# Kernel tuning notes

Hardware: AMD Instinct MI355X
Metric: run time of the kernel (lower is better)

Reference implementation:

```python
import jax, jax.numpy as jnp
import numpy as np

H, DH, C, K = 8, 128, 200, 15  # heads, head_dim, context_size, conv kernel
SCALE = DH ** -0.5
EPS = 1e-5


def layernorm(x, g, b):
    mu = jnp.mean(x, axis=-1, keepdims=True)
    var = jnp.mean(jnp.square(x - mu), axis=-1, keepdims=True)
    return (x - mu) * jax.lax.rsqrt(var + EPS) * g + b


def feedforward(x, ln_g, ln_b, up_w, up_b, down_w, down_b):
    h = layernorm(x, ln_g, ln_b)
    h = jax.nn.silu(h @ up_w + up_b)
    return h @ down_w + down_b


def attention(x, dist, ln_g, ln_b, wq, wkv, wo, wo_b, rel_emb):
    h = layernorm(x, ln_g, ln_b)
    b, f, d = h.shape
    nb = f // C  # num_features chosen divisible by context_size (no remainder path)
    q = (h @ wq).reshape(b, nb, C, H, DH).transpose(0, 1, 3, 2, 4)   # [b,nb,H,C,dh]
    kv = h @ wkv
    k, v = jnp.split(kv, 2, axis=-1)
    k = k.reshape(b, nb, C, H, DH).transpose(0, 1, 3, 2, 4)
    v = v.reshape(b, nb, C, H, DH).transpose(0, 1, 3, 2, 4)
    rel = rel_emb[dist]                                              # [C,C,dh]
    pos_attn = jnp.einsum('bnhid,ijd->bnhij', q, rel) * SCALE
    scores = jnp.einsum('bnhid,bnhjd->bnhij', q, k) * SCALE + pos_attn
    probs = jax.nn.softmax(scores, axis=-1)
    out = jnp.einsum('bnhij,bnhjd->bnhid', probs, v)
    out = out.transpose(0, 1, 3, 2, 4).reshape(b, f, H * DH)
    return out @ wo + wo_b


def conv_module(x, ln_g, ln_b, up_w, up_b, dw_w, bn_g, bn_b, bn_mean, bn_var, down_w, down_b):
    h = layernorm(x, ln_g, ln_b)
    h = h @ up_w + up_b                         # pointwise conv == linear; [b,L,2*inner]
    a, gate = jnp.split(h, 2, axis=-1)
    h = a * jax.nn.sigmoid(gate)                # GLU over channel dim
    h = h.transpose(0, 2, 1)                    # [b,inner,L]
    pad = K // 2
    h = jax.lax.conv_general_dilated(
        h, dw_w[:, None, :], window_strides=(1,), padding=[(pad, pad)],
        dimension_numbers=('NCH', 'OIH', 'NCH'), feature_group_count=h.shape[1])
    # BatchNorm1d in eval mode (running stats)
    h = (h - bn_mean[None, :, None]) * jax.lax.rsqrt(bn_var[None, :, None] + EPS)
    h = h * bn_g[None, :, None] + bn_b[None, :, None]
    h = jax.nn.silu(h)
    h = h.transpose(0, 2, 1) @ down_w + down_b  # [b,L,hidden]
    return h


def block_forward(x, attention_dists,
                  ff1_ln_g, ff1_ln_b, ff1_up_w, ff1_up_b, ff1_down_w, ff1_down_b,
                  attn_ln_g, attn_ln_b, wq, wkv, wo, wo_b, rel_emb,
                  conv_ln_g, conv_ln_b, conv_up_w, conv_up_b, dw_w,
                  bn_g, bn_b, bn_mean, bn_var, conv_down_w, conv_down_b,
                  ff2_ln_g, ff2_ln_b, ff2_up_w, ff2_up_b, ff2_down_w, ff2_down_b,
                  post_ln_g, post_ln_b):
    x = 0.5 * feedforward(x, ff1_ln_g, ff1_ln_b, ff1_up_w, ff1_up_b, ff1_down_w, ff1_down_b) + x
    x = attention(x, attention_dists, attn_ln_g, attn_ln_b, wq, wkv, wo, wo_b, rel_emb) + x
    x = conv_module(x, conv_ln_g, conv_ln_b, conv_up_w, conv_up_b, dw_w,
                    bn_g, bn_b, bn_mean, bn_var, conv_down_w, conv_down_b) + x
    x = 0.5 * feedforward(x, ff2_ln_g, ff2_ln_b, ff2_up_w, ff2_up_b, ff2_down_w, ff2_down_b) + x
    return layernorm(x, post_ln_g, post_ln_b)


def setup_inputs() -> dict:
    key = jax.random.key(0)
    ks = iter(jax.random.split(key, 40))
    d, dff, inner = 1024, 4096, 2048
    r = lambda shape, s=0.02: (jax.random.normal(next(ks), shape, jnp.float32) * s)
    inp = {
        'x': jax.random.normal(next(ks), (8, 2000, d), jnp.float32),
        'attention_dists': jax.random.randint(next(ks), (C, C), 0, 1025, jnp.int32),
        'ff1_ln_g': jnp.ones((d,)), 'ff1_ln_b': jnp.zeros((d,)),
        'ff1_up_w': r((d, dff)), 'ff1_up_b': jnp.zeros((dff,)),
        'ff1_down_w': r((dff, d)), 'ff1_down_b': jnp.zeros((d,)),
        'attn_ln_g': jnp.ones((d,)), 'attn_ln_b': jnp.zeros((d,)),
        'wq': r((d, H * DH)), 'wkv': r((d, 2 * H * DH)),
        'wo': r((H * DH, d)), 'wo_b': jnp.zeros((d,)),
        'rel_emb': r((2 * 512 + 1, DH)),
        'conv_ln_g': jnp.ones((d,)), 'conv_ln_b': jnp.zeros((d,)),
        'conv_up_w': r((d, 2 * inner)), 'conv_up_b': jnp.zeros((2 * inner,)),
        'dw_w': r((inner, K)),
        'bn_g': jnp.ones((inner,)), 'bn_b': jnp.zeros((inner,)),
        'bn_mean': r((inner,)), 'bn_var': jax.random.uniform(next(ks), (inner,), jnp.float32) + 0.5,
        'conv_down_w': r((inner, d)), 'conv_down_b': jnp.zeros((d,)),
        'ff2_ln_g': jnp.ones((d,)), 'ff2_ln_b': jnp.zeros((d,)),
        'ff2_up_w': r((d, dff)), 'ff2_up_b': jnp.zeros((dff,)),
        'ff2_down_w': r((dff, d)), 'ff2_down_b': jnp.zeros((d,)),
        'post_ln_g': jnp.ones((d,)), 'post_ln_b': jnp.zeros((d,)),
    }
    return inp


def reference(x, attention_dists,
              ff1_ln_g, ff1_ln_b, ff1_up_w, ff1_up_b, ff1_down_w, ff1_down_b,
              attn_ln_g, attn_ln_b, wq, wkv, wo, wo_b, rel_emb,
              conv_ln_g, conv_ln_b, conv_up_w, conv_up_b, dw_w,
              bn_g, bn_b, bn_mean, bn_var, conv_down_w, conv_down_b,
              ff2_ln_g, ff2_ln_b, ff2_up_w, ff2_up_b, ff2_down_w, ff2_down_b,
              post_ln_g, post_ln_b):
    return block_forward(x, attention_dists,
                         ff1_ln_g, ff1_ln_b, ff1_up_w, ff1_up_b, ff1_down_w, ff1_down_b,
                         attn_ln_g, attn_ln_b, wq, wkv, wo, wo_b, rel_emb,
                         conv_ln_g, conv_ln_b, conv_up_w, conv_up_b, dw_w,
                         bn_g, bn_b, bn_mean, bn_var, conv_down_w, conv_down_b,
                         ff2_ln_g, ff2_ln_b, ff2_up_w, ff2_up_b, ff2_down_w, ff2_down_b,
                         post_ln_g, post_ln_b)
```

## Files before the change

kernel.cpp:

```cpp
#include <hip/hip_runtime.h>

typedef unsigned short u16;
typedef unsigned int u32;
using short8 = __attribute__((ext_vector_type(8))) short;
using floatx4 = __attribute__((ext_vector_type(4))) float;

#define DMODEL 1024
#define DFF 4096
#define INNER 2048
#define DH 128
#define CTX 200
#define R_TOT 16000
#define ABN 40
#define AROWS (ABN * CTX)
#define AM (ABN * 8)
#define SCALE_Q 0.08838834764831845f

__device__ __forceinline__ u16 f2bf(float f) {
    union { float f; u32 u; } v; v.f = f;
    u32 r = v.u + 0x7FFFu + ((v.u >> 16) & 1u);
    return (u16)(r >> 16);
}
__device__ __forceinline__ float bf2f(u16 u) {
    union { u32 u; float f; } v; v.u = ((u32)u) << 16; return v.f;
}
__device__ __forceinline__ float sigmoidf_(float x) { return 1.f / (1.f + __expf(-x)); }

__device__ __forceinline__ void load_lds16(const void* g, void* l) {
    __builtin_amdgcn_global_load_lds((const __attribute__((address_space(1))) u32*)g,
                                     (__attribute__((address_space(3))) u32*)l, 16, 0, 0);
}

template <typename RowMap>
__device__ __forceinline__ void stage256(const char* __restrict__ src, RowMap rowoff, int nrows,
                                         int row0, int k0b, char* dst) {
    const int lane = threadIdx.x & 63;
    const int wave = threadIdx.x >> 6;
#pragma unroll
    for (int r = 0; r < 4; ++r) {
        int o = r * 8192 + wave * 1024 + lane * 16;
        int row = o >> 7;
        int srcb = (o & 127) ^ ((row & 7) << 4);
        int grow = row0 + row;
        grow = (grow < nrows) ? grow : (nrows - 1);
        const char* g = src + rowoff(grow) + k0b + srcb;
        load_lds16(g, dst + r * 8192 + wave * 1024);
    }
}

template <typename RMA, typename RMB, typename Epi>
__device__ __forceinline__ void gemm256_core(const char* __restrict__ A, RMA rma, int a_rows,
                                             const char* __restrict__ B, RMB rmb, int b_rows,
                                             int K, int row0, int col0, char* lds, Epi epi) {
    const int lane = threadIdx.x & 63;
    const int wave = threadIdx.x >> 6;
    const int wrow = (wave >> 2) * 128;
    const int wcol = (wave & 3) * 64;
    const int lr = lane & 15;
    const int kg = lane >> 4;
    const int nt = K >> 6;

    floatx4 acc[8][4];
#pragma unroll
    for (int i = 0; i < 8; ++i)
#pragma unroll
        for (int j = 0; j < 4; ++j) acc[i][j] = (floatx4){0.f, 0.f, 0.f, 0.f};

    stage256(A, rma, a_rows, row0, 0, lds);
    stage256(B, rmb, b_rows, col0, 0, lds + 32768);
    asm volatile("s_waitcnt vmcnt(0)" ::: "memory");
    __builtin_amdgcn_s_barrier();

    for (int t = 0; t < nt; ++t) {
        char* cur = lds + (t & 1) * 65536;
        char* nxt = lds + ((t + 1) & 1) * 65536;
        if (t + 1 < nt) {
            stage256(A, rma, a_rows, row0, (t + 1) << 7, nxt);
            stage256(B, rmb, b_rows, col0, (t + 1) << 7, nxt + 32768);
        }
#pragma unroll
        for (int ks = 0; ks < 2; ++ks) {
            short8 av[8], bv[4];
#pragma unroll
            for (int mi = 0; mi < 8; ++mi) {
                int row = wrow + mi * 16 + lr;
                int cb = (ks * 64 + kg * 16) ^ ((row & 7) << 4);
                av[mi] = *(const short8*)(cur + row * 128 + cb);
            }
#pragma unroll
            for (int ni = 0; ni < 4; ++ni) {
                int row = wcol + ni * 16 + lr;
                int cb = (ks * 64 + kg * 16) ^ ((row & 7) << 4);
                bv[ni] = *(const short8*)(cur + 32768 + row * 128 + cb);
            }
            __builtin_amdgcn_s_setprio(1);
#pragma unroll
            for (int mi = 0; mi < 8; ++mi)
#pragma unroll
                for (int ni = 0; ni < 4; ++ni)
                    acc[mi][ni] = __builtin_amdgcn_mfma_f32_16x16x32_bf16(av[mi], bv[ni],
                                                                          acc[mi][ni], 0, 0, 0);
            __builtin_amdgcn_s_setprio(0);
        }
        if (t + 1 < nt)
            asm volatile("s_waitcnt vmcnt(0) lgkmcnt(0)" ::: "memory");
        else
            asm volatile("s_waitcnt lgkmcnt(0)" ::: "memory");
        __builtin_amdgcn_sched_barrier(0);
        __builtin_amdgcn_s_barrier();
    }
#pragma unroll
    for (int mi = 0; mi < 8; ++mi)
#pragma unroll
        for (int ni = 0; ni < 4; ++ni)
#pragma unroll
            for (int rr = 0; rr < 4; ++rr)
                epi(row0 + wrow + mi * 16 + kg * 4 + rr, col0 + wcol + ni * 16 + lr,
                    acc[mi][ni][rr]);
}

__device__ __forceinline__ void xcd_stripe_remap(int& bx, int& by) {
    const int gx = gridDim.x;
    const int gxs = gx >> 3;
    const int id = blockIdx.y * gx + blockIdx.x;
    const int xcd = id & 7;
    const int local = id >> 3;
    bx = xcd * gxs + (local % gxs);
    by = local / gxs;
}

template <int MODE>
__global__ __launch_bounds__(512, 2) void k_gemm256(const u16* __restrict__ A, int lda,
                                                    const u16* __restrict__ Bt, int ldb,
                                                    const float* __restrict__ bias, float alpha,
                                                    void* out, int ldc, const float* resid,
                                                    int M, int N, int K) {
    __shared__ __align__(128) char lds[131072];
    int bx, by;
    xcd_stripe_remap(bx, by);
    const int row0 = bx * 256, col0 = by * 256;
    if (row0 >= M) return;
    u16* ob = (u16*)out;
    float* of = (float*)out;
    const size_t la = (size_t)lda * 2, lb = (size_t)ldb * 2;
    gemm256_core((const char*)A, [=](int r) { return (size_t)r * la; }, M,
                 (const char*)Bt, [=](int r) { return (size_t)r * lb; }, N, K, row0, col0, lds,
                 [&](int r, int c, float v) {
                     if (r >= M) return;
                     size_t idx = (size_t)r * ldc + c;
                     float bb = bias ? bias[c] : 0.f;
                     if (MODE == 0) {
                         ob[idx] = f2bf(alpha * v + bb);
                     } else if (MODE == 1) {
                         float t = v + bb;
                         ob[idx] = f2bf(t * sigmoidf_(t));
                     } else {
                         of[idx] = alpha * (v + bb) + resid[idx];
                     }
                 });
}

template <typename RowMap>
__device__ __forceinline__ void stage_tile_g(const char* __restrict__ src, RowMap rowoff,
                                             int nrows, int row0, int k0b, char* tile) {
    const int lane = threadIdx.x & 63;
    const int wave = threadIdx.x >> 6;
#pragma unroll
    for (int r = 0; r < 4; ++r) {
        int o = r * 4096 + wave * 1024 + lane * 16;
        int row = o >> 7;
        int srcb = (o & 127) ^ ((row & 7) << 4);
        int grow = row0 + row;
        grow = (grow < nrows) ? grow : (nrows - 1);
        const char* g = src + rowoff(grow) + k0b + srcb;
        load_lds16(g, tile + r * 4096 + wave * 1024);
    }
}

template <typename RMA, typename RMB, typename Epi>
__device__ __forceinline__ void gemm_core_g(const char* __restrict__ A, RMA rma, int a_rows,
                                            const char* __restrict__ B, RMB rmb, int b_rows,
                                            int K, int row0, int col0, char* lds, Epi epi) {
    const int lane = threadIdx.x & 63;
    const int wave = threadIdx.x >> 6;
    const int wrow = (wave >> 1) * 64;
    const int wcol = (wave & 1) * 64;
    const int lr = lane & 15;
    const int kg = lane >> 4;
    const int nt = K >> 6;

    floatx4 acc[4][4];
#pragma unroll
    for (int i = 0; i < 4; ++i)
#pragma unroll
        for (int j = 0; j < 4; ++j) acc[i][j] = (floatx4){0.f, 0.f, 0.f, 0.f};

    stage_tile_g(A, rma, a_rows, row0, 0, lds);
    stage_tile_g(B, rmb, b_rows, col0, 0, lds + 16384);
    asm volatile("s_waitcnt vmcnt(0)" ::: "memory");
    __builtin_amdgcn_s_barrier();

    for (int t = 0; t < nt; ++t) {
        char* cur = lds + (t & 1) * 32768;
        char* nxt = lds + ((t + 1) & 1) * 32768;
        if (t + 1 < nt) {
            stage_tile_g(A, rma, a_rows, row0, (t + 1) << 7, nxt);
            stage_tile_g(B, rmb, b_rows, col0, (t + 1) << 7, nxt + 16384);
        }
#pragma unroll
        for (int ks = 0; ks < 2; ++ks) {
            short8 av[4], bv[4];
#pragma unroll
            for (int mi = 0; mi < 4; ++mi) {
                int row = wrow + mi * 16 + lr;
                int cb = (ks * 64 + kg * 16) ^ ((row & 7) << 4);
                av[mi] = *(const short8*)(cur + row * 128 + cb);
            }
#pragma unroll
            for (int ni = 0; ni < 4; ++ni) {
                int row = wcol + ni * 16 + lr;
                int cb = (ks * 64 + kg * 16) ^ ((row & 7) << 4);
                bv[ni] = *(const short8*)(cur + 16384 + row * 128 + cb);
            }
            __builtin_amdgcn_s_setprio(1);
#pragma unroll
            for (int mi = 0; mi < 4; ++mi)
#pragma unroll
                for (int ni = 0; ni < 4; ++ni)
                    acc[mi][ni] = __builtin_amdgcn_mfma_f32_16x16x32_bf16(av[mi], bv[ni],
                                                                          acc[mi][ni], 0, 0, 0);
            __builtin_amdgcn_s_setprio(0);
        }
        if (t + 1 < nt)
            asm volatile("s_waitcnt vmcnt(0) lgkmcnt(0)" ::: "memory");
        else
            asm volatile("s_waitcnt lgkmcnt(0)" ::: "memory");
        __builtin_amdgcn_sched_barrier(0);
        __builtin_amdgcn_s_barrier();
    }
#pragma unroll
    for (int mi = 0; mi < 4; ++mi)
#pragma unroll
        for (int ni = 0; ni < 4; ++ni)
#pragma unroll
            for (int rr = 0; rr < 4; ++rr)
                epi(row0 + wrow + mi * 16 + kg * 4 + rr, col0 + wcol + ni * 16 + lr,
                    acc[mi][ni][rr]);
}

__global__ __launch_bounds__(256, 2) void k_qk(const u16* __restrict__ q,
                                               const u16* __restrict__ kvc,
                                               u16* __restrict__ sc, int bn0) {
    __shared__ __align__(128) char lds[65536];
    const int z = blockIdx.z, bnl = z >> 3, h = z & 7;
    const char* A = (const char*)(q + ((size_t)(bn0 + bnl) * CTX) * DMODEL + h * DH);
    const char* B = (const char*)(kvc + ((size_t)bnl * CTX) * (2 * DMODEL) + h * DH);
    u16* out = sc + (size_t)z * CTX * 256;
    gemm_core_g(A, [](int r) { return (size_t)r * (DMODEL * 2); }, CTX, B,
                [](int r) { return (size_t)r * (4 * DMODEL); }, CTX, DH, blockIdx.x * 128,
                blockIdx.y * 128, lds, [&](int r, int c, float v) {
                    if (r < CTX) out[(size_t)r * 256 + c] = f2bf(v);
                });
}

__global__ __launch_bounds__(256, 2) void k_pos(const u16* __restrict__ q,
                                                const u16* __restrict__ rel,
                                                u16* __restrict__ sc, int m0) {
    __shared__ __align__(128) char lds[65536];
    const int i = blockIdx.z;
    const char* B = (const char*)(rel + (size_t)i * CTX * DH);
    u16* out = sc + i * 256;
    gemm_core_g((const char*)q,
                [=](int r) {
                    int m = m0 + r;
                    return (size_t)(((m >> 3) * CTX + i) * DMODEL + (m & 7) * DH) * 2;
                },
                AM, B, [](int r) { return (size_t)r * (DH * 2); }, CTX, DH, blockIdx.x * 128,
                blockIdx.y * 128, lds, [&](int r, int c, float v) {
                    if (r < AM) {
                        size_t idx = (size_t)r * (CTX * 256) + c;
                        out[idx] = f2bf(bf2f(out[idx]) + v);
                    }
                });
}

__global__ __launch_bounds__(256, 2) void k_pv(const u16* __restrict__ P,
                                               const u16* __restrict__ vT,
                                               u16* __restrict__ attn, int bn0) {
    __shared__ __align__(128) char lds[65536];
    const int z = blockIdx.z;
    u16* out = attn + ((size_t)(bn0 + (z >> 3)) * CTX) * DMODEL + (z & 7) * DH;
    const char* A = (const char*)(P + (size_t)z * CTX * 256);
    const char* B = (const char*)(vT + (size_t)z * DH * 256);
    gemm_core_g(A, [](int r) { return (size_t)r * 512; }, CTX, B,
                [](int r) { return (size_t)r * 512; }, DH, 256, blockIdx.x * 128, 0, lds,
                [&](int r, int c, float v) {
                    if (r < CTX) out[(size_t)r * DMODEL + c] = f2bf(v);
                });
}

template <bool OUTF32>
__global__ __launch_bounds__(256) void k_ln(const float* __restrict__ x,
                                            const float* __restrict__ g,
                                            const float* __restrict__ b, void* __restrict__ out) {
    const int row = blockIdx.x, t = threadIdx.x, lane = t & 63, wv = t >> 6;
    const float4 v = ((const float4*)(x + (size_t)row * DMODEL))[t];
    float s = v.x + v.y + v.z + v.w;
    float q = v.x * v.x + v.y * v.y + v.z * v.z + v.w * v.w;
#pragma unroll
    for (int off = 32; off > 0; off >>= 1) { s += __shfl_down(s, off); q += __shfl_down(q, off); }
    __shared__ float rs_[4], rq_[4];
    if (lane == 0) { rs_[wv] = s; rq_[wv] = q; }
    __syncthreads();
    s = rs_[0] + rs_[1] + rs_[2] + rs_[3];
    q = rq_[0] + rq_[1] + rq_[2] + rq_[3];
    const float mu = s * (1.f / DMODEL);
    const float rstd = rsqrtf(q * (1.f / DMODEL) - mu * mu + 1e-5f);
    const float4 gv = ((const float4*)g)[t];
    const float4 bv = ((const float4*)b)[t];
    float o0 = (v.x - mu) * rstd * gv.x + bv.x;
    float o1 = (v.y - mu) * rstd * gv.y + bv.y;
    float o2 = (v.z - mu) * rstd * gv.z + bv.z;
    float o3 = (v.w - mu) * rstd * gv.w + bv.w;
    if (OUTF32) {
        ((float4*)out)[(size_t)row * 256 + t] = make_float4(o0, o1, o2, o3);
    } else {
        ushort4 r4;
        r4.x = f2bf(o0); r4.y = f2bf(o1); r4.z = f2bf(o2); r4.w = f2bf(o3);
        ((ushort4*)out)[(size_t)row * 256 + t] = r4;
    }
}

__global__ __launch_bounds__(256) void k_softmax(u16* __restrict__ sc) {
    const size_t row = blockIdx.x;
    const int t = threadIdx.x, lane = t & 63, wv = t >> 6;
    float v = (t < CTX) ? bf2f(sc[row * 256 + t]) : -3.0e38f;
    float m = v;
#pragma unroll
    for (int off = 32; off > 0; off >>= 1) m = fmaxf(m, __shfl_down(m, off));
    __shared__ float rm[4], rsum[4];
    if (lane == 0) rm[wv] = m;
    __syncthreads();
    m = fmaxf(fmaxf(rm[0], rm[1]), fmaxf(rm[2], rm[3]));
    float e = (t < CTX) ? __expf(v - m) : 0.f;
    float s = e;
#pragma unroll
    for (int off = 32; off > 0; off >>= 1) s += __shfl_down(s, off);
    if (lane == 0) rsum[wv] = s;
    __syncthreads();
    s = rsum[0] + rsum[1] + rsum[2] + rsum[3];
    sc[row * 256 + t] = f2bf(e / s);
}

__global__ __launch_bounds__(256) void k_glu(u16* __restrict__ mid) {
    const size_t r = blockIdx.x;
    const int c = threadIdx.x * 8;
    const short8 a8 = *(const short8*)(mid + r * 4096 + c);
    const short8 g8 = *(const short8*)(mid + r * 4096 + 2048 + c);
    short8 o8;
#pragma unroll
    for (int e = 0; e < 8; ++e) {
        float av = bf2f((u16)a8[e]), gg = bf2f((u16)g8[e]);
        o8[e] = (short)f2bf(av * sigmoidf_(gg));
    }
    *(short8*)(mid + r * 4096 + c) = o8;
}

__global__ __launch_bounds__(256) void k_dwconv(const u16* __restrict__ in,
                                                const float* __restrict__ w,
                                                const float* __restrict__ bng,
                                                const float* __restrict__ bnb,
                                                const float* __restrict__ bnm,
                                                const float* __restrict__ bnv,
                                                u16* __restrict__ out) {
    const int b = blockIdx.z, lt = blockIdx.x, cg = blockIdx.y;
    const int c = cg * 256 + threadIdx.x;
    const int l0 = lt * 16;
    __shared__ u16 s[30][256];
#pragma unroll
    for (int rr = 0; rr < 30; ++rr) {
        int l = l0 + rr - 7;
        u16 v = 0;
        if (l >= 0 && l < 2000) v = in[((size_t)b * 2000 + l) * 4096 + c];
        s[rr][threadIdx.x] = v;
    }
    __syncthreads();
    float wv[15];
#pragma unroll
    for (int k = 0; k < 15; ++k) wv[k] = w[c * 15 + k];
    const float sc = rsqrtf(bnv[c] + 1e-5f) * bng[c];
    const float mean = bnm[c], bb = bnb[c];
#pragma unroll
    for (int l = 0; l < 16; ++l) {
        float acc = 0.f;
#pragma unroll
        for (int k = 0; k < 15; ++k) acc += bf2f(s[l + k][threadIdx.x]) * wv[k];
        float h = (acc - mean) * sc + bb;
        h = h * sigmoidf_(h);
        out[((size_t)b * 2000 + l0 + l) * 4096 + c] = f2bf(h);
    }
}

__global__ __launch_bounds__(256) void k_wt(const float* __restrict__ w, u16* __restrict__ wt,
                                            int K, int N) {
    __shared__ float tile[32][33];
    const int k0 = blockIdx.x * 32, n0 = blockIdx.y * 32;
    const int tx = threadIdx.x & 31, ty = threadIdx.x >> 5;
#pragma unroll
    for (int i = 0; i < 32; i += 8) tile[ty + i][tx] = w[(size_t)(k0 + ty + i) * N + n0 + tx];
    __syncthreads();
#pragma unroll
    for (int i = 0; i < 32; i += 8)
        wt[(size_t)(n0 + ty + i) * K + k0 + tx] = f2bf(tile[tx][ty + i]);
}

__global__ void k_rel(const float* __restrict__ emb, const int* __restrict__ dist,
                      u16* __restrict__ rel) {
    const int bid = blockIdx.x;
    const int d = dist[bid];
    rel[(size_t)bid * DH + threadIdx.x] = f2bf(emb[(size_t)d * DH + threadIdx.x]);
}

__global__ __launch_bounds__(256) void k_vt(const u16* __restrict__ kvc, u16* __restrict__ vT) {
    __shared__ u16 t_[64 * 130];
    const int z = blockIdx.x, jt = blockIdx.y;
    const int bnl = z >> 3, h = z & 7;
    const int j0 = jt * 64;
    for (int idx = threadIdx.x; idx < 8192; idx += 256) {
        int j = idx >> 7, dh = idx & 127;
        int jj = j0 + j;
        u16 val = 0;
        if (jj < CTX) val = kvc[((size_t)(bnl * CTX + jj)) * (2 * DMODEL) + DMODEL + h * DH + dh];
        t_[j * 130 + dh] = val;
    }
    __syncthreads();
    for (int idx = threadIdx.x; idx < 8192; idx += 256) {
        int dh = idx >> 6, j = idx & 63;
        vT[((size_t)z * DH + dh) * 256 + j0 + j] = t_[j * 130 + dh];
    }
}

__global__ void k_fill(float* o, int n, float v) {
    int i = blockIdx.x * 256 + threadIdx.x;
    if (i < n) o[i] = v;
}

extern "C" void kernel_launch(void* const* d_in, const int* in_sizes, int n_in, void* d_out,
                              int out_size, void* d_ws, size_t ws_size, hipStream_t stream) {
    const float* x_in = (const float*)d_in[0];
    const int* dists = (const int*)d_in[1];
    const float* ff1_ln_g = (const float*)d_in[2];
    const float* ff1_ln_b = (const float*)d_in[3];
    const float* ff1_up_w = (const float*)d_in[4];
    const float* ff1_up_b = (const float*)d_in[5];
    const float* ff1_down_w = (const float*)d_in[6];
    const float* ff1_down_b = (const float*)d_in[7];
    const float* attn_ln_g = (const float*)d_in[8];
    const float* attn_ln_b = (const float*)d_in[9];
    const float* wq = (const float*)d_in[10];
    const float* wkv = (const float*)d_in[11];
    const float* wo = (const float*)d_in[12];
    const float* wo_b = (const float*)d_in[13];
    const float* rel_emb = (const float*)d_in[14];
    const float* conv_ln_g = (const float*)d_in[15];
    const float* conv_ln_b = (const float*)d_in[16];
    const float* conv_up_w = (const float*)d_in[17];
    const float* conv_up_b = (const float*)d_in[18];
    const float* dw_w = (const float*)d_in[19];
    const float* bn_g = (const float*)d_in[20];
    const float* bn_b = (const float*)d_in[21];
    const float* bn_mean = (const float*)d_in[22];
    const float* bn_var = (const float*)d_in[23];
    const float* conv_down_w = (const float*)d_in[24];
    const float* conv_down_b = (const float*)d_in[25];
    const float* ff2_ln_g = (const float*)d_in[26];
    const float* ff2_ln_b = (const float*)d_in[27];
    const float* ff2_up_w = (const float*)d_in[28];
    const float* ff2_up_b = (const float*)d_in[29];
    const float* ff2_down_w = (const float*)d_in[30];
    const float* ff2_down_b = (const float*)d_in[31];
    const float* post_ln_g = (const float*)d_in[32];
    const float* post_ln_b = (const float*)d_in[33];

    char* W = (char*)d_ws;
    size_t off = 0;
    auto alloc = [&](size_t bytes) {
        char* p = W + off;
        off += (bytes + 255) & ~(size_t)255;
        return (u16*)p;
    };
    u16* slot = alloc((size_t)4096 * 1024 * 2);
    u16* ln_buf = alloc((size_t)R_TOT * DMODEL * 2);
    u16* arena = alloc((size_t)R_TOT * DFF * 2);
    u16* mid = arena;
    u16* rel_bf = arena;
    u16* bufA = rel_bf + (size_t)CTX * CTX * DH;
    u16* bufB = bufA + (size_t)AROWS * 2 * DMODEL;
    u16* smid = bufB + (size_t)R_TOT * DMODEL;
    u16* vT = smid + (size_t)AM * CTX * 256;
    float* xs = (float*)d_out;

    if (ws_size < off) {
        k_fill<<<(out_size + 255) / 256, 256, 0, stream>>>((float*)d_out, out_size, 31337.f);
        return;
    }

    auto WT = [&](const float* s, int K, int N) {
        k_wt<<<dim3(K / 32, N / 32), 256, 0, stream>>>(s, slot, K, N);
    };

    const dim3 gUP(64, 16);
    const dim3 gSQ(64, 4);
    const dim3 gKV(32, 8);

    auto ff_block = [&](const float* lng, const float* lnb, const float* upw, const float* upb,
                        const float* dnw, const float* dnb, const float* resid,
                        const float* xsrc) {
        k_ln<false><<<R_TOT, 256, 0, stream>>>(xsrc, lng, lnb, ln_buf);
        WT(upw, 1024, 4096);
        k_gemm256<1><<<gUP, 512, 0, stream>>>(ln_buf, DMODEL, slot, DMODEL, upb, 1.f, mid, DFF,
                                              nullptr, R_TOT, DFF, DMODEL);
        WT(dnw, 4096, 1024);
        k_gemm256<2><<<gSQ, 512, 0, stream>>>(mid, DFF, slot, DFF, dnb, 0.5f, xs, DMODEL, resid,
                                              R_TOT, DMODEL, DFF);
    };

    ff_block(ff1_ln_g, ff1_ln_b, ff1_up_w, ff1_up_b, ff1_down_w, ff1_down_b, x_in, x_in);

    k_ln<false><<<R_TOT, 256, 0, stream>>>(xs, attn_ln_g, attn_ln_b, ln_buf);
    k_rel<<<CTX * CTX, 128, 0, stream>>>(rel_emb, dists, rel_bf);
    WT(wq, 1024, 1024);
    k_gemm256<0><<<gSQ, 512, 0, stream>>>(ln_buf, DMODEL, slot, DMODEL, nullptr, SCALE_Q, bufB,
                                          DMODEL, nullptr, R_TOT, DMODEL, DMODEL);
    WT(wkv, 1024, 2048);
    for (int h = 0; h < 2; ++h) {
        const int bn0 = h * ABN, m0 = bn0 * 8;
        const u16* lnc = ln_buf + (size_t)bn0 * CTX * DMODEL;
        k_gemm256<0><<<gKV, 512, 0, stream>>>(lnc, DMODEL, slot, DMODEL, nullptr, 1.f, bufA,
                                              2 * DMODEL, nullptr, AROWS, 2 * DMODEL, DMODEL);
        k_vt<<<dim3(AM, 4), 256, 0, stream>>>(bufA, vT);
        k_qk<<<dim3(2, 2, AM), 256, 0, stream>>>(bufB, bufA, smid, bn0);
        k_pos<<<dim3(3, 2, CTX), 256, 0, stream>>>(bufB, rel_bf, smid, m0);
        k_softmax<<<AM * CTX, 256, 0, stream>>>(smid);
        k_pv<<<dim3(2, 1, AM), 256, 0, stream>>>(smid, vT, bufB, bn0);
    }
    WT(wo, 1024, 1024);
    k_gemm256<2><<<gSQ, 512, 0, stream>>>(bufB, DMODEL, slot, DMODEL, wo_b, 1.f, xs, DMODEL, xs,
                                          R_TOT, DMODEL, DMODEL);

    k_ln<false><<<R_TOT, 256, 0, stream>>>(xs, conv_ln_g, conv_ln_b, ln_buf);
    WT(conv_up_w, 1024, 4096);
    k_gemm256<0><<<gUP, 512, 0, stream>>>(ln_buf, DMODEL, slot, DMODEL, conv_up_b, 1.f, mid, DFF,
                                          nullptr, R_TOT, DFF, DMODEL);
    k_glu<<<R_TOT, 256, 0, stream>>>(mid);
    k_dwconv<<<dim3(125, 8, 8), 256, 0, stream>>>(mid, dw_w, bn_g, bn_b, bn_mean, bn_var,
                                                  mid + INNER);
    WT(conv_down_w, 2048, 1024);
    k_gemm256<2><<<gSQ, 512, 0, stream>>>(mid + INNER, DFF, slot, INNER, conv_down_b, 1.f, xs,
                                          DMODEL, xs, R_TOT, DMODEL, INNER);

    ff_block(ff2_ln_g, ff2_ln_b, ff2_up_w, ff2_up_b, ff2_down_w, ff2_down_b, xs, xs);

    k_ln<true><<<R_TOT, 256, 0, stream>>>(xs, post_ln_g, post_ln_b, d_out);
}
```

Before: 1.957 ms.

## Triple-buffer B tiles and interleave half-tile staging with MFMA quarters

Restructures the 256x256 GEMM main loop. B tiles are now triple-buffered and prefetched two K-steps ahead, while A stays double-buffered. Global-to-LDS staging is split into half-tiles issued between four MFMA quarter-steps, and a partial vmcnt wait replaces the full drain at the end of each iteration. The goal is to hide global load latency behind compute, at the cost of raising LDS to 160KB per block and adding a workgroup barrier after each quarter.

```diff
diff --git a/kernel.cpp b/kernel.cpp
--- a/kernel.cpp
+++ b/kernel.cpp
@@ -32,19 +32,18 @@
 }
 
 template <typename RowMap>
-__device__ __forceinline__ void stage256(const char* __restrict__ src, RowMap rowoff, int nrows,
-                                         int row0, int k0b, char* dst) {
+__device__ __forceinline__ void stage_half(const char* __restrict__ src, RowMap rowoff,
+                                           int nrows, int row0, int k0b, char* slab, int half) {
     const int lane = threadIdx.x & 63;
     const int wave = threadIdx.x >> 6;
 #pragma unroll
-    for (int r = 0; r < 4; ++r) {
+    for (int r = 2 * half; r < 2 * half + 2; ++r) {
         int o = r * 8192 + wave * 1024 + lane * 16;
         int row = o >> 7;
         int srcb = (o & 127) ^ ((row & 7) << 4);
         int grow = row0 + row;
         grow = (grow < nrows) ? grow : (nrows - 1);
-        const char* g = src + rowoff(grow) + k0b + srcb;
-        load_lds16(g, dst + r * 8192 + wave * 1024);
+        load_lds16(src + rowoff(grow) + k0b + srcb, slab + r * 8192 + wave * 1024);
     }
 }
 
@@ -52,6 +51,8 @@
 __device__ __forceinline__ void gemm256_core(const char* __restrict__ A, RMA rma, int a_rows,
                                              const char* __restrict__ B, RMB rmb, int b_rows,
                                              int K, int row0, int col0, char* lds, Epi epi) {
+    char* ldsA = lds;
+    char* ldsB = lds + 65536;
     const int lane = threadIdx.x & 63;
     const int wave = threadIdx.x >> 6;
     const int wrow = (wave >> 2) * 128;
@@ -66,48 +67,71 @@
 #pragma unroll
         for (int j = 0; j < 4; ++j) acc[i][j] = (floatx4){0.f, 0.f, 0.f, 0.f};
 
-    stage256(A, rma, a_rows, row0, 0, lds);
-    stage256(B, rmb, b_rows, col0, 0, lds + 32768);
-    asm volatile("s_waitcnt vmcnt(0)" ::: "memory");
-    __builtin_amdgcn_s_barrier();
-
+    stage_half(B, rmb, b_rows, col0, 0, ldsB, 0);
+    stage_half(B, rmb, b_rows, col0, 0, ldsB, 1);
+    stage_half(A, rma, a_rows, row0, 0, ldsA, 0);
+    stage_half(A, rma, a_rows, row0, 0, ldsA, 1);
+    if (nt > 1) {
+        stage_half(B, rmb, b_rows, col0, 128, ldsB + 32768, 0);
+        stage_half(B, rmb, b_rows, col0, 128, ldsB + 32768, 1);
+    }
+
+    int bcur = 0;
     for (int t = 0; t < nt; ++t) {
-        char* cur = lds + (t & 1) * 65536;
-        char* nxt = lds + ((t + 1) & 1) * 65536;
-        if (t + 1 < nt) {
-            stage256(A, rma, a_rows, row0, (t + 1) << 7, nxt);
-            stage256(B, rmb, b_rows, col0, (t + 1) << 7, nxt + 32768);
+        char* curA = ldsA + (t & 1) * 32768;
+        char* curB = ldsB + bcur * 32768;
+        const int bnx2 = (bcur >= 1) ? bcur - 1 : 2;
+        if (t + 1 < nt)
+            asm volatile("s_waitcnt vmcnt(4)" ::: "memory");
+        else
+            asm volatile("s_waitcnt vmcnt(0)" ::: "memory");
+        __builtin_amdgcn_s_barrier();
+
+        short8 bv[4][2];
+#pragma unroll
+        for (int ni = 0; ni < 4; ++ni) {
+            int row = wcol + ni * 16 + lr;
+#pragma unroll
+            for (int ks = 0; ks < 2; ++ks) {
+                int cb = (ks * 64 + kg * 16) ^ ((row & 7) << 4);
+                bv[ni][ks] = *(const short8*)(curB + row * 128 + cb);
+            }
         }
 #pragma unroll
-        for (int ks = 0; ks < 2; ++ks) {
-            short8 av[8], bv[4];
-#pragma unroll
-            for (int mi = 0; mi < 8; ++mi) {
-                int row = wrow + mi * 16 + lr;
-                int cb = (ks * 64 + kg * 16) ^ ((row & 7) << 4);
-                av[mi] = *(const short8*)(cur + row * 128 + cb);
+        for (int q = 0; q < 4; ++q) {
+            short8 av[2][2];
+#pragma unroll
+            for (int m2 = 0; m2 < 2; ++m2) {
+                int row = wrow + (2 * q + m2) * 16 + lr;
+#pragma unroll
+                for (int ks = 0; ks < 2; ++ks) {
+                    int cb = (ks * 64 + kg * 16) ^ ((row & 7) << 4);
+                    av[m2][ks] = *(const short8*)(curA + row * 128 + cb);
+                }
             }
-#pragma unroll
-            for (int ni = 0; ni < 4; ++ni) {
-                int row = wcol + ni * 16 + lr;
-                int cb = (ks * 64 + kg * 16) ^ ((row & 7) << 4);
-                bv[ni] = *(const short8*)(cur + 32768 + row * 128 + cb);
-            }
+            if (q == 0 && t + 1 < nt)
+                stage_half(A, rma, a_rows, row0, (t + 1) << 7, ldsA + ((t + 1) & 1) * 32768, 0);
+            if (q == 1 && t + 1 < nt)
+                stage_half(A, rma, a_rows, row0, (t + 1) << 7, ldsA + ((t + 1) & 1) * 32768, 1);
+            if (q == 2 && t + 2 < nt)
+                stage_half(B, rmb, b_rows, col0, (t + 2) << 7, ldsB + bnx2 * 32768, 0);
+            if (q == 3 && t + 2 < nt)
+                stage_half(B, rmb, b_rows, col0, (t + 2) << 7, ldsB + bnx2 * 32768, 1);
+            asm volatile("s_waitcnt lgkmcnt(0)" ::: "memory");
+            __builtin_amdgcn_sched_barrier(0);
             __builtin_amdgcn_s_setprio(1);
 #pragma unroll
-            for (int mi = 0; mi < 8; ++mi)
-#pragma unroll
-                for (int ni = 0; ni < 4; ++ni)
-                    acc[mi][ni] = __builtin_amdgcn_mfma_f32_16x16x32_bf16(av[mi], bv[ni],
-                                                                          acc[mi][ni], 0, 0, 0);
+            for (int ks = 0; ks < 2; ++ks)
+#pragma unroll
+                for (int m2 = 0; m2 < 2; ++m2)
+#pragma unroll
+                    for (int ni = 0; ni < 4; ++ni)
+                        acc[2 * q + m2][ni] = __builtin_amdgcn_mfma_f32_16x16x32_bf16(
+                            av[m2][ks], bv[ni][ks], acc[2 * q + m2][ni], 0, 0, 0);
             __builtin_amdgcn_s_setprio(0);
+            __builtin_amdgcn_s_barrier();
         }
-        if (t + 1 < nt)
-            asm volatile("s_waitcnt vmcnt(0) lgkmcnt(0)" ::: "memory");
-        else
-            asm volatile("s_waitcnt lgkmcnt(0)" ::: "memory");
-        __builtin_amdgcn_sched_barrier(0);
-        __builtin_amdgcn_s_barrier();
+        bcur = (bcur >= 2) ? 0 : bcur + 1;
     }
 #pragma unroll
     for (int mi = 0; mi < 8; ++mi)
@@ -135,7 +159,7 @@
                                                     const float* __restrict__ bias, float alpha,
                                                     void* out, int ldc, const float* resid,
                                                     int M, int N, int K) {
-    __shared__ __align__(128) char lds[131072];
+    __shared__ __align__(128) char lds[163840];
     int bx, by;
     xcd_stripe_remap(bx, by);
     const int row0 = bx * 256, col0 = by * 256;
```

Result: no change. 1.940 ms (-0.9%).

## Replace 256x256 double-buffered GEMM with simpler 128x128 single-buffered kernel

Applied to the files above, without the earlier changes.

Swaps the 512-thread, 256x256-tile GEMM that double-buffers 128KB of LDS for a 256-thread, 128x128-tile kernel with a single 32KB LDS buffer, precomputed source pointers and three blocks per CU. Grids are doubled in each dimension to match. The aim is more resident blocks and less LDS pressure. In exchange it drops load/compute overlap inside a block, since each k-step waits for its loads, and halves data reuse per tile.

```diff
diff --git a/kernel.cpp b/kernel.cpp
--- a/kernel.cpp
+++ b/kernel.cpp
@@ -31,94 +31,6 @@
                                      (__attribute__((address_space(3))) u32*)l, 16, 0, 0);
 }
 
-template <typename RowMap>
-__device__ __forceinline__ void stage256(const char* __restrict__ src, RowMap rowoff, int nrows,
-                                         int row0, int k0b, char* dst) {
-    const int lane = threadIdx.x & 63;
-    const int wave = threadIdx.x >> 6;
-#pragma unroll
-    for (int r = 0; r < 4; ++r) {
-        int o = r * 8192 + wave * 1024 + lane * 16;
-        int row = o >> 7;
-        int srcb = (o & 127) ^ ((row & 7) << 4);
-        int grow = row0 + row;
-        grow = (grow < nrows) ? grow : (nrows - 1);
-        const char* g = src + rowoff(grow) + k0b + srcb;
-        load_lds16(g, dst + r * 8192 + wave * 1024);
-    }
-}
-
-template <typename RMA, typename RMB, typename Epi>
-__device__ __forceinline__ void gemm256_core(const char* __restrict__ A, RMA rma, int a_rows,
-                                             const char* __restrict__ B, RMB rmb, int b_rows,
-                                             int K, int row0, int col0, char* lds, Epi epi) {
-    const int lane = threadIdx.x & 63;
-    const int wave = threadIdx.x >> 6;
-    const int wrow = (wave >> 2) * 128;
-    const int wcol = (wave & 3) * 64;
-    const int lr = lane & 15;
-    const int kg = lane >> 4;
-    const int nt = K >> 6;
-
-    floatx4 acc[8][4];
-#pragma unroll
-    for (int i = 0; i < 8; ++i)
-#pragma unroll
-        for (int j = 0; j < 4; ++j) acc[i][j] = (floatx4){0.f, 0.f, 0.f, 0.f};
-
-    stage256(A, rma, a_rows, row0, 0, lds);
-    stage256(B, rmb, b_rows, col0, 0, lds + 32768);
-    asm volatile("s_waitcnt vmcnt(0)" ::: "memory");
-    __builtin_amdgcn_s_barrier();
-
-    for (int t = 0; t < nt; ++t) {
-        char* cur = lds + (t & 1) * 65536;
-        char* nxt = lds + ((t + 1) & 1) * 65536;
-        if (t + 1 < nt) {
-            stage256(A, rma, a_rows, row0, (t + 1) << 7, nxt);
-            stage256(B, rmb, b_rows, col0, (t + 1) << 7, nxt + 32768);
-        }
-#pragma unroll
-        for (int ks = 0; ks < 2; ++ks) {
-            short8 av[8], bv[4];
-#pragma unroll
-            for (int mi = 0; mi < 8; ++mi) {
-                int row = wrow + mi * 16 + lr;
-                int cb = (ks * 64 + kg * 16) ^ ((row & 7) << 4);
-                av[mi] = *(const short8*)(cur + row * 128 + cb);
-            }
-#pragma unroll
-            for (int ni = 0; ni < 4; ++ni) {
-                int row = wcol + ni * 16 + lr;
-                int cb = (ks * 64 + kg * 16) ^ ((row & 7) << 4);
-                bv[ni] = *(const short8*)(cur + 32768 + row * 128 + cb);
-            }
-            __builtin_amdgcn_s_setprio(1);
-#pragma unroll
-            for (int mi = 0; mi < 8; ++mi)
-#pragma unroll
-                for (int ni = 0; ni < 4; ++ni)
-                    acc[mi][ni] = __builtin_amdgcn_mfma_f32_16x16x32_bf16(av[mi], bv[ni],
-                                                                          acc[mi][ni], 0, 0, 0);
-            __builtin_amdgcn_s_setprio(0);
-        }
-        if (t + 1 < nt)
-            asm volatile("s_waitcnt vmcnt(0) lgkmcnt(0)" ::: "memory");
-        else
-            asm volatile("s_waitcnt lgkmcnt(0)" ::: "memory");
-        __builtin_amdgcn_sched_barrier(0);
-        __builtin_amdgcn_s_barrier();
-    }
-#pragma unroll
-    for (int mi = 0; mi < 8; ++mi)
-#pragma unroll
-        for (int ni = 0; ni < 4; ++ni)
-#pragma unroll
-            for (int rr = 0; rr < 4; ++rr)
-                epi(row0 + wrow + mi * 16 + kg * 4 + rr, col0 + wcol + ni * 16 + lr,
-                    acc[mi][ni][rr]);
-}
-
 __device__ __forceinline__ void xcd_stripe_remap(int& bx, int& by) {
     const int gx = gridDim.x;
     const int gxs = gx >> 3;
@@ -130,34 +42,103 @@
 }
 
 template <int MODE>
-__global__ __launch_bounds__(512, 2) void k_gemm256(const u16* __restrict__ A, int lda,
-                                                    const u16* __restrict__ Bt, int ldb,
-                                                    const float* __restrict__ bias, float alpha,
-                                                    void* out, int ldc, const float* resid,
-                                                    int M, int N, int K) {
-    __shared__ __align__(128) char lds[131072];
+__device__ __forceinline__ void epi_store(int r, int c, float v, int M, int ldc,
+                                          const float* bias, float alpha, void* out,
+                                          const float* resid) {
+    if (r >= M) return;
+    size_t idx = (size_t)r * ldc + c;
+    float bb = bias ? bias[c] : 0.f;
+    if (MODE == 0) {
+        ((u16*)out)[idx] = f2bf(alpha * v + bb);
+    } else if (MODE == 1) {
+        float t = v + bb;
+        ((u16*)out)[idx] = f2bf(t * sigmoidf_(t));
+    } else {
+        ((float*)out)[idx] = alpha * (v + bb) + resid[idx];
+    }
+}
+
+template <int MODE>
+__global__ __launch_bounds__(256, 3) void k_g(const u16* __restrict__ A, int lda,
+                                              const u16* __restrict__ Bt, int ldb,
+                                              const float* __restrict__ bias, float alpha,
+                                              void* out, int ldc, const float* resid, int M,
+                                              int N, int K) {
+    __shared__ __align__(128) char lds[32768];
     int bx, by;
     xcd_stripe_remap(bx, by);
-    const int row0 = bx * 256, col0 = by * 256;
+    const int row0 = bx * 128, col0 = by * 128;
     if (row0 >= M) return;
-    u16* ob = (u16*)out;
-    float* of = (float*)out;
-    const size_t la = (size_t)lda * 2, lb = (size_t)ldb * 2;
-    gemm256_core((const char*)A, [=](int r) { return (size_t)r * la; }, M,
-                 (const char*)Bt, [=](int r) { return (size_t)r * lb; }, N, K, row0, col0, lds,
-                 [&](int r, int c, float v) {
-                     if (r >= M) return;
-                     size_t idx = (size_t)r * ldc + c;
-                     float bb = bias ? bias[c] : 0.f;
-                     if (MODE == 0) {
-                         ob[idx] = f2bf(alpha * v + bb);
-                     } else if (MODE == 1) {
-                         float t = v + bb;
-                         ob[idx] = f2bf(t * sigmoidf_(t));
-                     } else {
-                         of[idx] = alpha * (v + bb) + resid[idx];
-                     }
-                 });
+    const int lane = threadIdx.x & 63;
+    const int wave = threadIdx.x >> 6;
+    const int wrow = (wave >> 1) * 64;
+    const int wcol = (wave & 1) * 64;
+    const int lr = lane & 15;
+    const int kg = lane >> 4;
+    const int nt = K >> 6;
+
+    const char* sA[4];
+    const char* sB[4];
+#pragma unroll
+    for (int r = 0; r < 4; ++r) {
+        int o = r * 4096 + wave * 1024 + lane * 16;
+        int row = o >> 7;
+        int srcb = (o & 127) ^ ((row & 7) << 4);
+        int ga = row0 + row;
+        ga = (ga < M) ? ga : M - 1;
+        sA[r] = (const char*)A + (size_t)ga * ((size_t)lda * 2) + srcb;
+        int gb = col0 + row;
+        gb = (gb < N) ? gb : N - 1;
+        sB[r] = (const char*)Bt + (size_t)gb * ((size_t)ldb * 2) + srcb;
+    }
+    floatx4 acc[4][4];
+#pragma unroll
+    for (int i = 0; i < 4; ++i)
+#pragma unroll
+        for (int j = 0; j < 4; ++j) acc[i][j] = (floatx4){0.f, 0.f, 0.f, 0.f};
+
+    for (int t = 0; t < nt; ++t) {
+        const int kb = t << 7;
+#pragma unroll
+        for (int r = 0; r < 4; ++r) {
+            load_lds16(sA[r] + kb, lds + r * 4096 + wave * 1024);
+            load_lds16(sB[r] + kb, lds + 16384 + r * 4096 + wave * 1024);
+        }
+        asm volatile("s_waitcnt vmcnt(0)" ::: "memory");
+        __builtin_amdgcn_s_barrier();
+#pragma unroll
+        for (int ks = 0; ks < 2; ++ks) {
+            short8 av[4], bv[4];
+#pragma unroll
+            for (int mi = 0; mi < 4; ++mi) {
+                int row = wrow + mi * 16 + lr;
+                int cb = (ks * 64 + kg * 16) ^ ((row & 7) << 4);
+                av[mi] = *(const short8*)(lds + row * 128 + cb);
+            }
+#pragma unroll
+            for (int ni = 0; ni < 4; ++ni) {
+                int row = wcol + ni * 16 + lr;
+                int cb = (ks * 64 + kg * 16) ^ ((row & 7) << 4);
+                bv[ni] = *(const short8*)(lds + 16384 + row * 128 + cb);
+            }
+#pragma unroll
+            for (int mi = 0; mi < 4; ++mi)
+#pragma unroll
+                for (int ni = 0; ni < 4; ++ni)
+                    acc[mi][ni] = __builtin_amdgcn_mfma_f32_16x16x32_bf16(av[mi], bv[ni],
+                                                                          acc[mi][ni], 0, 0, 0);
+        }
+        asm volatile("s_waitcnt lgkmcnt(0)" ::: "memory");
+        __builtin_amdgcn_s_barrier();
+    }
+#pragma unroll
+    for (int mi = 0; mi < 4; ++mi)
+#pragma unroll
+        for (int ni = 0; ni < 4; ++ni)
+#pragma unroll
+            for (int rr = 0; rr < 4; ++rr)
+                epi_store<MODE>(row0 + wrow + mi * 16 + kg * 4 + rr, col0 + wcol + ni * 16 + lr,
+                                acc[mi][ni][rr], M, ldc, bias, alpha, out, resid);
 }
 
 template <typename RowMap>
@@ -509,20 +490,20 @@
         k_wt<<<dim3(K / 32, N / 32), 256, 0, stream>>>(s, slot, K, N);
     };
 
-    const dim3 gUP(64, 16);
-    const dim3 gSQ(64, 4);
-    const dim3 gKV(32, 8);
+    const dim3 gUP(128, 32);
+    const dim3 gSQ(128, 8);
+    const dim3 gKV(64, 16);
 
     auto ff_block = [&](const float* lng, const float* lnb, const float* upw, const float* upb,
                         const float* dnw, const float* dnb, const float* resid,
                         const float* xsrc) {
         k_ln<false><<<R_TOT, 256, 0, stream>>>(xsrc, lng, lnb, ln_buf);
         WT(upw, 1024, 4096);
-        k_gemm256<1><<<gUP, 512, 0, stream>>>(ln_buf, DMODEL, slot, DMODEL, upb, 1.f, mid, DFF,
-                                              nullptr, R_TOT, DFF, DMODEL);
+        k_g<1><<<gUP, 256, 0, stream>>>(ln_buf, DMODEL, slot, DMODEL, upb, 1.f, mid, DFF,
+                                        nullptr, R_TOT, DFF, DMODEL);
         WT(dnw, 4096, 1024);
-        k_gemm256<2><<<gSQ, 512, 0, stream>>>(mid, DFF, slot, DFF, dnb, 0.5f, xs, DMODEL, resid,
-                                              R_TOT, DMODEL, DFF);
+        k_g<2><<<gSQ, 256, 0, stream>>>(mid, DFF, slot, DFF, dnb, 0.5f, xs, DMODEL, resid,
+                                        R_TOT, DMODEL, DFF);
     };
 
     ff_block(ff1_ln_g, ff1_ln_b, ff1_up_w, ff1_up_b, ff1_down_w, ff1_down_b, x_in, x_in);
@@ -530,14 +511,14 @@
     k_ln<false><<<R_TOT, 256, 0, stream>>>(xs, attn_ln_g, attn_ln_b, ln_buf);
     k_rel<<<CTX * CTX, 128, 0, stream>>>(rel_emb, dists, rel_bf);
     WT(wq, 1024, 1024);
-    k_gemm256<0><<<gSQ, 512, 0, stream>>>(ln_buf, DMODEL, slot, DMODEL, nullptr, SCALE_Q, bufB,
-                                          DMODEL, nullptr, R_TOT, DMODEL, DMODEL);
+    k_g<0><<<gSQ, 256, 0, stream>>>(ln_buf, DMODEL, slot, DMODEL, nullptr, SCALE_Q, bufB,
+                                    DMODEL, nullptr, R_TOT, DMODEL, DMODEL);
     WT(wkv, 1024, 2048);
     for (int h = 0; h < 2; ++h) {
         const int bn0 = h * ABN, m0 = bn0 * 8;
         const u16* lnc = ln_buf + (size_t)bn0 * CTX * DMODEL;
-        k_gemm256<0><<<gKV, 512, 0, stream>>>(lnc, DMODEL, slot, DMODEL, nullptr, 1.f, bufA,
-                                              2 * DMODEL, nullptr, AROWS, 2 * DMODEL, DMODEL);
+        k_g<0><<<gKV, 256, 0, stream>>>(lnc, DMODEL, slot, DMODEL, nullptr, 1.f, bufA,
+                                        2 * DMODEL, nullptr, AROWS, 2 * DMODEL, DMODEL);
         k_vt<<<dim3(AM, 4), 256, 0, stream>>>(bufA, vT);
         k_qk<<<dim3(2, 2, AM), 256, 0, stream>>>(bufB, bufA, smid, bn0);
         k_pos<<<dim3(3, 2, CTX), 256, 0, stream>>>(bufB, rel_bf, smid, m0);
@@ -545,19 +526,19 @@
         k_pv<<<dim3(2, 1, AM), 256, 0, stream>>>(smid, vT, bufB, bn0);
     }
     WT(wo, 1024, 1024);
-    k_gemm256<2><<<gSQ, 512, 0, stream>>>(bufB, DMODEL, slot, DMODEL, wo_b, 1.f, xs, DMODEL, xs,
-                                          R_TOT, DMODEL, DMODEL);
+    k_g<2><<<gSQ, 256, 0, stream>>>(bufB, DMODEL, slot, DMODEL, wo_b, 1.f, xs, DMODEL, xs,
+                                    R_TOT, DMODEL, DMODEL);
 
     k_ln<false><<<R_TOT, 256, 0, stream>>>(xs, conv_ln_g, conv_ln_b, ln_buf);
     WT(conv_up_w, 1024, 4096);
-    k_gemm256<0><<<gUP, 512, 0, stream>>>(ln_buf, DMODEL, slot, DMODEL, conv_up_b, 1.f, mid, DFF,
-                                          nullptr, R_TOT, DFF, DMODEL);
+    k_g<0><<<gUP, 256, 0, stream>>>(ln_buf, DMODEL, slot, DMODEL, conv_up_b, 1.f, mid, DFF,
+                                    nullptr, R_TOT, DFF, DMODEL);
     k_glu<<<R_TOT, 256, 0, stream>>>(mid);
     k_dwconv<<<dim3(125, 8, 8), 256, 0, stream>>>(mid, dw_w, bn_g, bn_b, bn_mean, bn_var,
                                                   mid + INNER);
     WT(conv_down_w, 2048, 1024);
-    k_gemm256<2><<<gSQ, 512, 0, stream>>>(mid + INNER, DFF, slot, INNER, conv_down_b, 1.f, xs,
-                                          DMODEL, xs, R_TOT, DMODEL, INNER);
+    k_g<2><<<gSQ, 256, 0, stream>>>(mid + INNER, DFF, slot, INNER, conv_down_b, 1.f, xs,
+                                    DMODEL, xs, R_TOT, DMODEL, INNER);
 
     ff_block(ff2_ln_g, ff2_ln_b, ff2_up_w, ff2_up_b, ff2_down_w, ff2_down_b, xs, xs);
 
```

New measurement: 1.704 ms. -12.9%, faster.
